# Optimization experiments

Measured on AMD Instinct MI355X. Metric: run time of the kernel, lower is better.

The kernel has to match this reference:

```python
import jax, jax.numpy as jnp
import numpy as np

B, F, T, D = 8, 256, 32, 1024
NEG = -1e30


def setup_inputs() -> dict:
    key = jax.random.key(0)
    ks = jax.random.split(key, 10)
    s = 1.0 / np.sqrt(D)
    return {
        "features": jax.random.normal(ks[0], (B, F, D), jnp.float32),
        "masks": jnp.ones((B, F), jnp.float32),  # unused by the module
        "textual_features": jax.random.normal(ks[1], (B, T, D), jnp.float32),
        "q_masks": jax.random.randint(ks[2], (B, T), 0, 2, jnp.int32),
        "Ws": jax.random.normal(ks[3], (D, D), jnp.float32) * s,
        "W": jax.random.normal(ks[4], (D, D), jnp.float32) * s,
        "w": jax.random.normal(ks[5], (D, 1), jnp.float32) * s,
        "b": jax.random.normal(ks[6], (1, D), jnp.float32) * s,
        "Wcw": jax.random.normal(ks[7], (1, D), jnp.float32) * s,
        "bcw": jnp.zeros((1,), jnp.float32),
        "Wcb": jax.random.normal(ks[8], (1, D), jnp.float32) * s,
        "bcb": jnp.zeros((1,), jnp.float32),
    }


def reference(features, masks, textual_features, q_masks, Ws, W, w, b, Wcw, bcw, Wcb, bcb):
    # Vectorized over all f_len frames at once (original loops over k).
    txt_proj = jnp.einsum("btd,de->bte", textual_features, Ws)   # [B,T,D]
    feat_proj = jnp.einsum("bfd,de->bfe", features, W)           # [B,F,D]
    # additive-attention hidden: [B,F,T,D]
    h = jnp.tanh(txt_proj[:, None, :, :] + feat_proj[:, :, None, :] + b[None, None, :, :][..., 0, :])
    rho = jnp.einsum("bftd,d->bft", h, w[:, 0])                  # [B,F,T]
    qm = q_masks.astype(jnp.float32)
    rho = rho + (1.0 - qm)[:, None, :] * NEG                     # mask_logits
    att = jax.nn.softmax(rho, axis=-1)                          # over t_len
    txt_h = jnp.einsum("bft,btd->bfd", att, textual_features)    # [B,F,D]
    w_s = jnp.tanh(jnp.einsum("bfd,od->bfo", txt_h, Wcw) + bcw)  # [B,F,1]
    b_s = jnp.tanh(jnp.einsum("bfd,od->bfo", txt_h, Wcb) + bcb)  # [B,F,1]
    return w_s * features + b_s
```

## Files before the change

kernel.cpp:

```cpp
#include <hip/hip_runtime.h>
#include <math.h>

#define Bdim 8
#define Fdim 256
#define Tdim 32
#define Ddim 1024
#define NEGV (-1e30f)
#define TANH_SCALE 2.8853900817779268f
#define LOG2E 1.4426950408889634f

typedef unsigned short ushort;
using short8  = __attribute__((ext_vector_type(8))) short;
using floatx4 = __attribute__((ext_vector_type(4))) float;

__device__ __forceinline__ float fexp2(float x) { return __builtin_amdgcn_exp2f(x); }
__device__ __forceinline__ float frcp(float x)  { return __builtin_amdgcn_rcpf(x); }

__device__ __forceinline__ float fast_tanh(float x) {
    return 1.0f - 2.0f * frcp(fexp2(x * TANH_SCALE) + 1.0f);
}

__device__ __forceinline__ ushort f2bf(float f) {
    unsigned u = __float_as_uint(f);
    unsigned r = u + 0x7FFFu + ((u >> 16) & 1u);
    return (ushort)(r >> 16);
}

#define GLOAD_LDS16(gp, lp) __builtin_amdgcn_global_load_lds(                   \
    (const __attribute__((address_space(1))) void*)(gp),                        \
    (__attribute__((address_space(3))) void*)(lp), 16, 0, 0)

__global__ __launch_bounds__(256) void prep(
    const float* __restrict__ feat, const float* __restrict__ txt,
    const float* __restrict__ W, const float* __restrict__ Ws,
    ushort* __restrict__ featB, ushort* __restrict__ txtB,
    ushort* __restrict__ WtB, ushort* __restrict__ WstB)
{
    __shared__ ushort tile[32][33];
    const int blk = blockIdx.x;
    const int NCAST = Bdim * Fdim + Bdim * Tdim;
    if (blk < NCAST) {
        const float* in; ushort* out; int base;
        if (blk < Bdim * Fdim) { in = feat; out = featB; base = blk * Ddim; }
        else { in = txt; out = txtB; base = (blk - Bdim * Fdim) * Ddim; }
        const int i = base + threadIdx.x * 4;
        float4 v = *(const float4*)(in + i);
        ushort4 o;
        o.x = f2bf(v.x); o.y = f2bf(v.y); o.z = f2bf(v.z); o.w = f2bf(v.w);
        *(ushort4*)(out + i) = o;
    } else {
        int t = blk - NCAST;
        const float* in = (t < 1024) ? W : Ws;
        ushort* out = (t < 1024) ? WtB : WstB;
        t &= 1023;
        const int bx = (t & 31) * 32;
        const int by = (t >> 5) * 32;
        const int tx = threadIdx.x & 31;
        const int tg = threadIdx.x >> 5;
        #pragma unroll
        for (int r = tg; r < 32; r += 8)
            tile[r][tx] = f2bf(in[(size_t)(by + r) * Ddim + bx + tx]);
        __syncthreads();
        #pragma unroll
        for (int r = tg; r < 32; r += 8)
            out[(size_t)(bx + r) * Ddim + by + tx] = tile[tx][r];
    }
}

#define GBM 128
#define GBN 64
#define GBK 32

__global__ __launch_bounds__(256) void gemm_dual(
    const ushort* __restrict__ A1, const ushort* __restrict__ Bt1, float* __restrict__ C1,
    const ushort* __restrict__ A2, const ushort* __restrict__ Bt2, float* __restrict__ C2,
    const float* __restrict__ bias2)
{
    const int K = Ddim, N = Ddim;
    const int by = blockIdx.y;
    const ushort* A; const ushort* Bt; float* C; const float* bias; int m0;
    if (by < 16) { A = A1; Bt = Bt1; C = C1; bias = nullptr; m0 = by * GBM; }
    else         { A = A2; Bt = Bt2; C = C2; bias = bias2;  m0 = (by - 16) * GBM; }
    const int n0 = blockIdx.x * GBN;

    __shared__ __align__(16) ushort As[GBM * GBK];
    __shared__ __align__(16) ushort Bs[GBN * GBK];

    const int tid  = threadIdx.x;
    const int l    = tid & 63;
    const int wave = tid >> 6;

    const int crow = l >> 2;
    const int ccol = (l & 3) * 8;

    const int wm = (wave >> 1) * 64;
    const int wn = (wave & 1) * 32;

    floatx4 acc[4][2];
    #pragma unroll
    for (int i = 0; i < 4; ++i)
        #pragma unroll
        for (int j = 0; j < 2; ++j)
            acc[i][j] = (floatx4){0.0f, 0.0f, 0.0f, 0.0f};

    const int lm = l & 15;
    const int lk = (l >> 4) * 8;

    const ushort* aSrc0 = A  + (size_t)(m0 + wave * 16       + crow) * K + ccol;
    const ushort* aSrc1 = A  + (size_t)(m0 + (wave + 4) * 16 + crow) * K + ccol;
    const ushort* bSrc  = Bt + (size_t)(n0 + wave * 16       + crow) * K + ccol;
    ushort* aDst0 = &As[(wave * 16) * GBK];
    ushort* aDst1 = &As[((wave + 4) * 16) * GBK];
    ushort* bDst  = &Bs[(wave * 16) * GBK];

    for (int k0 = 0; k0 < K; k0 += GBK) {
        __syncthreads();
        GLOAD_LDS16(aSrc0 + k0, aDst0);
        GLOAD_LDS16(aSrc1 + k0, aDst1);
        GLOAD_LDS16(bSrc  + k0, bDst);
        __syncthreads();

        short8 af0 = *(const short8*)&As[(wm +  0 + lm) * GBK + lk];
        short8 af1 = *(const short8*)&As[(wm + 16 + lm) * GBK + lk];
        short8 af2 = *(const short8*)&As[(wm + 32 + lm) * GBK + lk];
        short8 af3 = *(const short8*)&As[(wm + 48 + lm) * GBK + lk];
        short8 bf0 = *(const short8*)&Bs[(wn +  0 + lm) * GBK + lk];
        short8 bf1 = *(const short8*)&Bs[(wn + 16 + lm) * GBK + lk];
        acc[0][0] = __builtin_amdgcn_mfma_f32_16x16x32_bf16(af0, bf0, acc[0][0], 0, 0, 0);
        acc[0][1] = __builtin_amdgcn_mfma_f32_16x16x32_bf16(af0, bf1, acc[0][1], 0, 0, 0);
        acc[1][0] = __builtin_amdgcn_mfma_f32_16x16x32_bf16(af1, bf0, acc[1][0], 0, 0, 0);
        acc[1][1] = __builtin_amdgcn_mfma_f32_16x16x32_bf16(af1, bf1, acc[1][1], 0, 0, 0);
        acc[2][0] = __builtin_amdgcn_mfma_f32_16x16x32_bf16(af2, bf0, acc[2][0], 0, 0, 0);
        acc[2][1] = __builtin_amdgcn_mfma_f32_16x16x32_bf16(af2, bf1, acc[2][1], 0, 0, 0);
        acc[3][0] = __builtin_amdgcn_mfma_f32_16x16x32_bf16(af3, bf0, acc[3][0], 0, 0, 0);
        acc[3][1] = __builtin_amdgcn_mfma_f32_16x16x32_bf16(af3, bf1, acc[3][1], 0, 0, 0);
    }

    const int rowq = (l >> 4) * 4;
    #pragma unroll
    for (int im = 0; im < 4; ++im) {
        #pragma unroll
        for (int in_ = 0; in_ < 2; ++in_) {
            const int col = n0 + wn + in_ * 16 + lm;
            float badd = (bias != nullptr) ? bias[col] : 0.0f;
            #pragma unroll
            for (int r = 0; r < 4; ++r) {
                const int row = m0 + wm + im * 16 + rowq + r;
                C[(size_t)row * N + col] = (acc[im][in_][r] + badd) * TANH_SCALE;
            }
        }
    }
}

__global__ __launch_bounds__(256, 4) void attn_fused(
    const float* __restrict__ feat,
    const float* __restrict__ txt,
    const int*   __restrict__ qmask,
    const float* __restrict__ fp_s,
    const float* __restrict__ tp_s,
    const float* __restrict__ wvec,
    const float* __restrict__ Wcw,
    const float* __restrict__ bcw,
    const float* __restrict__ Wcb,
    const float* __restrict__ bcb,
    float* __restrict__ out)
{
    const int blk  = blockIdx.x;
    const int f0   = blk * 2;
    const int b    = f0 >> 8;
    const int tid  = threadIdx.x;
    const int lane = tid & 63;
    const int wave = tid >> 6;

    __shared__ float part[2][Tdim][68];
    __shared__ float srho[2][Tdim];
    __shared__ float satt[2][Tdim];
    __shared__ float sred[4][4];

    float4 wv[4], fva[4], fvb[4];
    const float* fr0 = fp_s + (size_t)f0 * Ddim;
    const float* fr1 = fr0 + Ddim;
    #pragma unroll
    for (int it = 0; it < 4; ++it) {
        const int d = lane * 4 + it * 256;
        wv[it]  = *(const float4*)&wvec[d];
        fva[it] = *(const float4*)&fr0[d];
        fvb[it] = *(const float4*)&fr1[d];
    }
    float sumw = 0.0f;
    #pragma unroll
    for (int it = 0; it < 4; ++it)
        sumw += wv[it].x + wv[it].y + wv[it].z + wv[it].w;
    #pragma unroll
    for (int off = 32; off; off >>= 1) sumw += __shfl_xor(sumw, off, 64);

    const float* tpb = tp_s + (size_t)b * Tdim * Ddim;
    float s0[8], s1[8];
    float4 cur[4], nxt[4];
    {
        const float* tr = tpb + (size_t)(wave * 8) * Ddim;
        #pragma unroll
        for (int it = 0; it < 4; ++it)
            cur[it] = *(const float4*)&tr[lane * 4 + it * 256];
    }
    #pragma unroll
    for (int tt = 0; tt < 8; ++tt) {
        if (tt < 7) {
            const float* trn = tpb + (size_t)(wave * 8 + tt + 1) * Ddim;
            #pragma unroll
            for (int it = 0; it < 4; ++it)
                nxt[it] = *(const float4*)&trn[lane * 4 + it * 256];
        }
        float a0 = 0.0f, b0 = 0.0f, a1 = 0.0f, b1 = 0.0f;
        #pragma unroll
        for (int it = 0; it < 4; ++it) {
            float4 tv = cur[it];
            float e, r;
            e = fexp2(tv.x + fva[it].x); r = frcp(e + 1.0f); a0 = fmaf(wv[it].x, r, a0);
            e = fexp2(tv.y + fva[it].y); r = frcp(e + 1.0f); b0 = fmaf(wv[it].y, r, b0);
            e = fexp2(tv.z + fva[it].z); r = frcp(e + 1.0f); a0 = fmaf(wv[it].z, r, a0);
            e = fexp2(tv.w + fva[it].w); r = frcp(e + 1.0f); b0 = fmaf(wv[it].w, r, b0);
            e = fexp2(tv.x + fvb[it].x); r = frcp(e + 1.0f); a1 = fmaf(wv[it].x, r, a1);
            e = fexp2(tv.y + fvb[it].y); r = frcp(e + 1.0f); b1 = fmaf(wv[it].y, r, b1);
            e = fexp2(tv.z + fvb[it].z); r = frcp(e + 1.0f); a1 = fmaf(wv[it].z, r, a1);
            e = fexp2(tv.w + fvb[it].w); r = frcp(e + 1.0f); b1 = fmaf(wv[it].w, r, b1);
        }
        s0[tt] = a0 + b0;
        s1[tt] = a1 + b1;
        #pragma unroll
        for (int it = 0; it < 4; ++it) cur[it] = nxt[it];
    }
    #pragma unroll
    for (int tt = 0; tt < 8; ++tt) {
        part[0][wave * 8 + tt][lane] = s0[tt];
        part[1][wave * 8 + tt][lane] = s1[tt];
    }
    __syncthreads();

    {
        const int pair = tid >> 2, q = tid & 3;
        const int f = pair >> 5, t = pair & 31;
        const float* src = &part[f][t][q * 16];
        float4 v0 = *(const float4*)(src);
        float4 v1 = *(const float4*)(src + 4);
        float4 v2 = *(const float4*)(src + 8);
        float4 v3 = *(const float4*)(src + 12);
        float sum = ((v0.x + v0.y) + (v0.z + v0.w))
                  + ((v1.x + v1.y) + (v1.z + v1.w))
                  + ((v2.x + v2.y) + (v2.z + v2.w))
                  + ((v3.x + v3.y) + (v3.z + v3.w));
        sum += __shfl_xor(sum, 1, 64);
        sum += __shfl_xor(sum, 2, 64);
        if (q == 0) srho[f][t] = sum;
    }
    __syncthreads();

    if (wave == 0) {
        const int f = lane >> 5, t = lane & 31;
        const float q = (float)qmask[b * Tdim + t];
        float L = sumw - 2.0f * srho[f][t] + (1.0f - q) * NEGV;
        float m = L;
        #pragma unroll
        for (int off = 16; off; off >>= 1) m = fmaxf(m, __shfl_xor(m, off, 64));
        float e = fexp2((L - m) * LOG2E);
        float ssum = e;
        #pragma unroll
        for (int off = 16; off; off >>= 1) ssum += __shfl_xor(ssum, off, 64);
        satt[f][t] = e * frcp(ssum);
    }
    __syncthreads();

    const float* txtb = txt + (size_t)b * Tdim * Ddim;
    const int d0 = tid * 4;
    float4 th0 = {0,0,0,0}, th1 = {0,0,0,0};
    #pragma unroll 8
    for (int t = 0; t < Tdim; ++t) {
        float4 tv = *(const float4*)&txtb[(size_t)t * Ddim + d0];
        const float a0 = satt[0][t], a1 = satt[1][t];
        th0.x = fmaf(a0, tv.x, th0.x); th0.y = fmaf(a0, tv.y, th0.y);
        th0.z = fmaf(a0, tv.z, th0.z); th0.w = fmaf(a0, tv.w, th0.w);
        th1.x = fmaf(a1, tv.x, th1.x); th1.y = fmaf(a1, tv.y, th1.y);
        th1.z = fmaf(a1, tv.z, th1.z); th1.w = fmaf(a1, tv.w, th1.w);
    }

    float4 wcw = *(const float4*)&Wcw[d0];
    float4 wcb = *(const float4*)&Wcb[d0];
    float p00 = th0.x*wcw.x + th0.y*wcw.y + th0.z*wcw.z + th0.w*wcw.w;
    float p01 = th0.x*wcb.x + th0.y*wcb.y + th0.z*wcb.z + th0.w*wcb.w;
    float p10 = th1.x*wcw.x + th1.y*wcw.y + th1.z*wcw.z + th1.w*wcw.w;
    float p11 = th1.x*wcb.x + th1.y*wcb.y + th1.z*wcb.z + th1.w*wcb.w;
    #pragma unroll
    for (int off = 32; off; off >>= 1) {
        p00 += __shfl_xor(p00, off, 64);
        p01 += __shfl_xor(p01, off, 64);
        p10 += __shfl_xor(p10, off, 64);
        p11 += __shfl_xor(p11, off, 64);
    }
    if (lane == 0) {
        sred[wave][0] = p00; sred[wave][1] = p01;
        sred[wave][2] = p10; sred[wave][3] = p11;
    }
    __syncthreads();
    const float c00 = sred[0][0] + sred[1][0] + sred[2][0] + sred[3][0];
    const float c01 = sred[0][1] + sred[1][1] + sred[2][1] + sred[3][1];
    const float c10 = sred[0][2] + sred[1][2] + sred[2][2] + sred[3][2];
    const float c11 = sred[0][3] + sred[1][3] + sred[2][3] + sred[3][3];
    const float ws0 = fast_tanh(c00 + bcw[0]);
    const float bs0 = fast_tanh(c01 + bcb[0]);
    const float ws1 = fast_tanh(c10 + bcw[0]);
    const float bs1 = fast_tanh(c11 + bcb[0]);

    const float* ft0 = feat + (size_t)f0 * Ddim;
    float4 v0 = *(const float4*)&ft0[d0];
    float4 v1 = *(const float4*)&ft0[Ddim + d0];
    float4 o0, o1;
    o0.x = fmaf(ws0, v0.x, bs0); o0.y = fmaf(ws0, v0.y, bs0);
    o0.z = fmaf(ws0, v0.z, bs0); o0.w = fmaf(ws0, v0.w, bs0);
    o1.x = fmaf(ws1, v1.x, bs1); o1.y = fmaf(ws1, v1.y, bs1);
    o1.z = fmaf(ws1, v1.z, bs1); o1.w = fmaf(ws1, v1.w, bs1);
    *(float4*)&out[(size_t)f0 * Ddim + d0] = o0;
    *(float4*)&out[(size_t)f0 * Ddim + Ddim + d0] = o1;
}

extern "C" void kernel_launch(void* const* d_in, const int* in_sizes, int n_in,
                              void* d_out, int out_size, void* d_ws, size_t ws_size,
                              hipStream_t stream) {
    const float* features = (const float*)d_in[0];
    const float* textual  = (const float*)d_in[2];
    const int*   q_masks  = (const int*)d_in[3];
    const float* Ws       = (const float*)d_in[4];
    const float* W        = (const float*)d_in[5];
    const float* wvec     = (const float*)d_in[6];
    const float* bvec     = (const float*)d_in[7];
    const float* Wcw      = (const float*)d_in[8];
    const float* bcw      = (const float*)d_in[9];
    const float* Wcb      = (const float*)d_in[10];
    const float* bcb      = (const float*)d_in[11];
    float* out = (float*)d_out;

    float*  fp_ws = (float*)d_ws;
    float*  tp_ws = fp_ws + (size_t)Bdim * Fdim * Ddim;
    ushort* featB = (ushort*)(tp_ws + (size_t)Bdim * Tdim * Ddim);
    ushort* txtB  = featB + (size_t)Bdim * Fdim * Ddim;
    ushort* WtB   = txtB + (size_t)Bdim * Tdim * Ddim;
    ushort* WstB  = WtB + (size_t)Ddim * Ddim;

    prep<<<Bdim * Fdim + Bdim * Tdim + 2048, 256, 0, stream>>>(
        features, textual, W, Ws, featB, txtB, WtB, WstB);
    gemm_dual<<<dim3(Ddim / GBN, 18), 256, 0, stream>>>(
        featB, WtB, fp_ws, txtB, WstB, tp_ws, bvec);
    attn_fused<<<(Bdim * Fdim) / 2, 256, 0, stream>>>(
        features, textual, q_masks, fp_ws, tp_ws,
        wvec, Wcw, bcw, Wcb, bcb, out);
}
```

Measured before the change: 128.1 us.

## Double-buffer LDS tiles in dual GEMM with vmcnt-based waits

```diff
diff --git a/kernel.cpp b/kernel.cpp
--- a/kernel.cpp
+++ b/kernel.cpp
@@ -29,6 +29,8 @@
 #define GLOAD_LDS16(gp, lp) __builtin_amdgcn_global_load_lds(                   \
     (const __attribute__((address_space(1))) void*)(gp),                        \
     (__attribute__((address_space(3))) void*)(lp), 16, 0, 0)
+
+#define WAIT_VMCNT(n) __builtin_amdgcn_s_waitcnt(((n) & 0xF) | (7 << 4) | (15 << 8) | (((n) >> 4) << 14))
 
 __global__ __launch_bounds__(256) void prep(
     const float* __restrict__ feat, const float* __restrict__ txt,
@@ -83,49 +85,62 @@
     else         { A = A2; Bt = Bt2; C = C2; bias = bias2;  m0 = (by - 16) * GBM; }
     const int n0 = blockIdx.x * GBN;
 
-    __shared__ __align__(16) ushort As[GBM * GBK];
-    __shared__ __align__(16) ushort Bs[GBN * GBK];
+    __shared__ __align__(16) ushort As[2][GBM * GBK];
+    __shared__ __align__(16) ushort Bs[2][GBN * GBK];
 
     const int tid  = threadIdx.x;
     const int l    = tid & 63;
     const int wave = tid >> 6;
 
+    const int wm = (wave >> 1) * 64;
+    const int wn = (wave & 1) * 32;
+
+    floatx4 acc[4][2];
+    #pragma unroll
+    for (int i = 0; i < 4; ++i)
+        #pragma unroll
+        for (int j = 0; j < 2; ++j)
+            acc[i][j] = (floatx4){0.0f, 0.0f, 0.0f, 0.0f};
+
+    const int lm = l & 15;
+    const int lk = (l >> 4) * 8;
+
     const int crow = l >> 2;
     const int ccol = (l & 3) * 8;
-
-    const int wm = (wave >> 1) * 64;
-    const int wn = (wave & 1) * 32;
-
-    floatx4 acc[4][2];
-    #pragma unroll
-    for (int i = 0; i < 4; ++i)
-        #pragma unroll
-        for (int j = 0; j < 2; ++j)
-            acc[i][j] = (floatx4){0.0f, 0.0f, 0.0f, 0.0f};
-
-    const int lm = l & 15;
-    const int lk = (l >> 4) * 8;
 
     const ushort* aSrc0 = A  + (size_t)(m0 + wave * 16       + crow) * K + ccol;
     const ushort* aSrc1 = A  + (size_t)(m0 + (wave + 4) * 16 + crow) * K + ccol;
     const ushort* bSrc  = Bt + (size_t)(n0 + wave * 16       + crow) * K + ccol;
-    ushort* aDst0 = &As[(wave * 16) * GBK];
-    ushort* aDst1 = &As[((wave + 4) * 16) * GBK];
-    ushort* bDst  = &Bs[(wave * 16) * GBK];
-
-    for (int k0 = 0; k0 < K; k0 += GBK) {
-        __syncthreads();
-        GLOAD_LDS16(aSrc0 + k0, aDst0);
-        GLOAD_LDS16(aSrc1 + k0, aDst1);
-        GLOAD_LDS16(bSrc  + k0, bDst);
-        __syncthreads();
-
-        short8 af0 = *(const short8*)&As[(wm +  0 + lm) * GBK + lk];
-        short8 af1 = *(const short8*)&As[(wm + 16 + lm) * GBK + lk];
-        short8 af2 = *(const short8*)&As[(wm + 32 + lm) * GBK + lk];
-        short8 af3 = *(const short8*)&As[(wm + 48 + lm) * GBK + lk];
-        short8 bf0 = *(const short8*)&Bs[(wn +  0 + lm) * GBK + lk];
-        short8 bf1 = *(const short8*)&Bs[(wn + 16 + lm) * GBK + lk];
+    const int aOff0 = (wave * 16) * GBK;
+    const int aOff1 = ((wave + 4) * 16) * GBK;
+    const int bOff  = (wave * 16) * GBK;
+
+    const int NK = K / GBK;
+
+    GLOAD_LDS16(aSrc0, &As[0][aOff0]);
+    GLOAD_LDS16(aSrc1, &As[0][aOff1]);
+    GLOAD_LDS16(bSrc,  &Bs[0][bOff]);
+
+    for (int i = 0; i < NK; ++i) {
+        const int cur = i & 1;
+        if (i + 1 < NK) {
+            const int kn = (i + 1) * GBK;
+            const int nxt = cur ^ 1;
+            GLOAD_LDS16(aSrc0 + kn, &As[nxt][aOff0]);
+            GLOAD_LDS16(aSrc1 + kn, &As[nxt][aOff1]);
+            GLOAD_LDS16(bSrc  + kn, &Bs[nxt][bOff]);
+            WAIT_VMCNT(3);
+        } else {
+            WAIT_VMCNT(0);
+        }
+        __builtin_amdgcn_s_barrier();
+
+        short8 af0 = *(const short8*)&As[cur][(wm +  0 + lm) * GBK + lk];
+        short8 af1 = *(const short8*)&As[cur][(wm + 16 + lm) * GBK + lk];
+        short8 af2 = *(const short8*)&As[cur][(wm + 32 + lm) * GBK + lk];
+        short8 af3 = *(const short8*)&As[cur][(wm + 48 + lm) * GBK + lk];
+        short8 bf0 = *(const short8*)&Bs[cur][(wn +  0 + lm) * GBK + lk];
+        short8 bf1 = *(const short8*)&Bs[cur][(wn + 16 + lm) * GBK + lk];
         acc[0][0] = __builtin_amdgcn_mfma_f32_16x16x32_bf16(af0, bf0, acc[0][0], 0, 0, 0);
         acc[0][1] = __builtin_amdgcn_mfma_f32_16x16x32_bf16(af0, bf1, acc[0][1], 0, 0, 0);
         acc[1][0] = __builtin_amdgcn_mfma_f32_16x16x32_bf16(af1, bf0, acc[1][0], 0, 0, 0);
@@ -134,6 +149,8 @@
         acc[2][1] = __builtin_amdgcn_mfma_f32_16x16x32_bf16(af2, bf1, acc[2][1], 0, 0, 0);
         acc[3][0] = __builtin_amdgcn_mfma_f32_16x16x32_bf16(af3, bf0, acc[3][0], 0, 0, 0);
         acc[3][1] = __builtin_amdgcn_mfma_f32_16x16x32_bf16(af3, bf1, acc[3][1], 0, 0, 0);
+
+        __builtin_amdgcn_s_barrier();
     }
 
     const int rowq = (l >> 4) * 4;
```

Result: no change. 127.4 us (-0.6%).
